# Performance work log

Measured on AMD Instinct MI355X. Metric: run time of the kernel, lower is better.

The kernel has to match this reference:

```python
import jax, jax.numpy as jnp
import numpy as np

N = 16384
F_IN = 256
F_OUT = 256


def setup_inputs() -> dict:
    key = jax.random.key(0)
    k1, k2, k3 = jax.random.split(key, 3)
    x = jax.random.normal(k1, (N, F_IN), dtype=jnp.float32)
    # dense 0/1 adjacency (original masks with adj[j] == 1)
    adj = jax.random.randint(k2, (N, N), 0, 2, dtype=jnp.int32)
    # glorot-uniform init for weight [2F_in, F_out]
    stdv = np.sqrt(6.0 / (2 * F_IN + F_OUT)).astype(np.float32)
    weight = jax.random.uniform(k3, (2 * F_IN, F_OUT), dtype=jnp.float32,
                                minval=-stdv, maxval=stdv)
    bias = jnp.zeros((F_OUT,), dtype=jnp.float32)
    return {"x": x, "adj": adj, "weight": weight, "bias": bias}


def reference(x, adj, weight, bias):
    # Mean over neighbors (adj row == 1): segment-mean expressed as a
    # normalized dense matmul -- equivalent to the per-row boolean-mask mean.
    a = adj.astype(x.dtype)                      # [N, N]
    deg = jnp.sum(a, axis=1, keepdims=True)      # [N, 1]
    x1 = (a @ x) / deg                           # [N, F] neighbor mean
    n_x = jnp.concatenate([x1, x], axis=1)       # [N, 2F]
    return n_x @ weight + bias                   # [N, F_out]
```

## Files before the change

### kernel.cpp

```cpp
#include <hip/hip_runtime.h>
#include <hip/hip_bf16.h>
#include <stdint.h>


typedef short bf16x8 __attribute__((ext_vector_type(8)));
typedef float f32x4  __attribute__((ext_vector_type(4)));

__device__ __forceinline__ uint32_t pack_bf16_rne(float lo, float hi) {
    uint32_t ul = __float_as_uint(lo);
    uint32_t uh = __float_as_uint(hi);
    ul = (ul + 0x7fffu + ((ul >> 16) & 1u)) >> 16;
    uh = (uh + 0x7fffu + ((uh >> 16) & 1u)) >> 16;
    return ul | (uh << 16);
}

__device__ __forceinline__ void gload_lds16(const void* g, void* l) {
    __builtin_amdgcn_global_load_lds(
        (__attribute__((address_space(1))) void*)g,
        (__attribute__((address_space(3))) void*)l, 16, 0, 0);
}

__global__ __launch_bounds__(256) void k_transpose_w(const float* __restrict__ w,
                                                     uint16_t* __restrict__ wt) {
    int idx = blockIdx.x * 256 + threadIdx.x;
    int n = idx >> 8;
    int k = idx & 255;
    int row = (n < 256) ? k : (256 + k);
    int col = (n < 256) ? n : (n - 256);
    uint32_t u = __float_as_uint(w[row * 256 + col]);
    u = (u + 0x7fffu + ((u >> 16) & 1u)) >> 16;
    wt[idx] = (uint16_t)u;
}

__global__ __launch_bounds__(256) void k_small_gemm(const float* __restrict__ x,
                                                    const uint16_t* __restrict__ wt,
                                                    const float* __restrict__ bias,
                                                    uint16_t* __restrict__ yT,
                                                    float* __restrict__ z) {
    __shared__ uint16_t As[128 * 32];
    __shared__ uint16_t Bs[128 * 32];

    const int t  = threadIdx.x;
    const int ct = blockIdx.x;
    const int rt = blockIdx.y;
    const int m0 = rt * 128;
    const int n0 = ct * 128;

    const int lane = t & 63, w = t >> 6;
    const int wr = w >> 1, wc = w & 1;
    const int l15 = lane & 15, quad = lane >> 4;

    f32x4 acc[4][4] = {};

    float4 a_reg[4];
    uint4  b_reg[2];

#pragma unroll
    for (int i = 0; i < 4; ++i) {
        int f4 = t + 256 * i, row = f4 >> 3, c4 = f4 & 7;
        a_reg[i] = *(const float4*)(x + (m0 + row) * 256 + c4 * 4);
    }
#pragma unroll
    for (int i = 0; i < 2; ++i) {
        int u4 = t + 256 * i, n_l = u4 >> 2, part = u4 & 3;
        b_reg[i] = *(const uint4*)(wt + (n0 + n_l) * 256 + part * 8);
    }

    for (int kk = 0; kk < 8; ++kk) {
        __syncthreads();
#pragma unroll
        for (int i = 0; i < 4; ++i) {
            int f4 = t + 256 * i, row = f4 >> 3, c4 = f4 & 7;
            uint2 p;
            p.x = pack_bf16_rne(a_reg[i].x, a_reg[i].y);
            p.y = pack_bf16_rne(a_reg[i].z, a_reg[i].w);
            *(uint2*)(As + row * 32 + c4 * 4) = p;
        }
#pragma unroll
        for (int i = 0; i < 2; ++i) {
            int u4 = t + 256 * i, n_l = u4 >> 2, part = u4 & 3;
            *(uint4*)(Bs + n_l * 32 + part * 8) = b_reg[i];
        }
        if (kk < 7) {
            int k0 = (kk + 1) * 32;
#pragma unroll
            for (int i = 0; i < 4; ++i) {
                int f4 = t + 256 * i, row = f4 >> 3, c4 = f4 & 7;
                a_reg[i] = *(const float4*)(x + (m0 + row) * 256 + k0 + c4 * 4);
            }
#pragma unroll
            for (int i = 0; i < 2; ++i) {
                int u4 = t + 256 * i, n_l = u4 >> 2, part = u4 & 3;
                b_reg[i] = *(const uint4*)(wt + (n0 + n_l) * 256 + k0 + part * 8);
            }
        }
        __syncthreads();

        bf16x8 a_frag[4], b_frag[4];
#pragma unroll
        for (int fr = 0; fr < 4; ++fr)
            a_frag[fr] = *(const bf16x8*)(As + (wr * 64 + fr * 16 + l15) * 32 + quad * 8);
#pragma unroll
        for (int fc = 0; fc < 4; ++fc)
            b_frag[fc] = *(const bf16x8*)(Bs + (wc * 64 + fc * 16 + l15) * 32 + quad * 8);
#pragma unroll
        for (int fr = 0; fr < 4; ++fr)
#pragma unroll
            for (int fc = 0; fc < 4; ++fc)
                acc[fr][fc] = __builtin_amdgcn_mfma_f32_16x16x32_bf16(
                    a_frag[fr], b_frag[fc], acc[fr][fc], 0, 0, 0);
    }

    if (ct < 2) {
#pragma unroll
        for (int fr = 0; fr < 4; ++fr) {
            int m_base = m0 + wr * 64 + fr * 16 + quad * 4;
#pragma unroll
            for (int fc = 0; fc < 4; ++fc) {
                int n_g = n0 + wc * 64 + fc * 16 + l15;
                uint2 pp;
                pp.x = pack_bf16_rne(acc[fr][fc][0], acc[fr][fc][1]);
                pp.y = pack_bf16_rne(acc[fr][fc][2], acc[fr][fc][3]);
                *(uint2*)(yT + (size_t)n_g * 16384 + m_base) = pp;
            }
        }
    } else {
#pragma unroll
        for (int fr = 0; fr < 4; ++fr) {
            int m_base = m0 + wr * 64 + fr * 16 + quad * 4;
#pragma unroll
            for (int fc = 0; fc < 4; ++fc) {
                int n_g = (n0 - 256) + wc * 64 + fc * 16 + l15;
                float bv = bias[n_g];
#pragma unroll
                for (int r = 0; r < 4; ++r)
                    z[(size_t)(m_base + r) * 256 + n_g] = acc[fr][fc][r] + bv;
            }
        }
    }
}

#define A_STRIDE 40
#define A_SZ (64 * A_STRIDE)
#define B_SZ (256 * 32)
#define KITER 256
__global__ __launch_bounds__(512, 4) void k_big_gemm(const int* __restrict__ adj,
                                                     const uint16_t* __restrict__ yT,
                                                     float* __restrict__ part,
                                                     int* __restrict__ degw) {
    __shared__ uint16_t As_f[2 * A_SZ];
    __shared__ uint16_t Bs_f[2 * B_SZ];

    const int t = threadIdx.x;
    const int m0 = blockIdx.x * 64;
    const int ky = blockIdx.y;
    const int kbase = ky * 8192;
    const int lane = t & 63, w = t >> 6;
    const int wr = w >> 2, wc = w & 3;
    const int l15 = lane & 15, quad = lane >> 4;

    f32x4 acc[2][4] = {};

    const int a_n = t >> 3, a_c4 = t & 7;
    const int4* pa4 = (const int4*)(adj + (size_t)(m0 + a_n) * 16384 + kbase) + a_c4;
    const int a_lds = a_n * A_STRIDE + a_c4 * 4;

    const uint16_t* pbg[2];
    int b_ldsbase[2];
#pragma unroll
    for (int i = 0; i < 2; ++i) {
        int base = (w * 2 + i) * 64;
        int s = base + lane;
        int bn = s >> 2;
        int bc = (s & 3) ^ ((bn >> 1) & 3);
        pbg[i] = yT + (size_t)bn * 16384 + kbase + bc * 8;
        b_ldsbase[i] = base * 8;
    }

    int4 aP = pa4[0];
    int4 aB = pa4[8];
    pa4 += 16;
#pragma unroll
    for (int i = 0; i < 2; ++i) {
        gload_lds16(pbg[i], &Bs_f[b_ldsbase[i]]);
        pbg[i] += 32;
    }
    int degp = aP.x + aP.y + aP.z + aP.w;
    {
        uint2 pv;
        pv.x = (uint32_t)(aP.x | (aP.y << 16)) * 0x3F80u;
        pv.y = (uint32_t)(aP.z | (aP.w << 16)) * 0x3F80u;
        *(uint2*)&As_f[a_lds] = pv;
    }
    __syncthreads();

    for (int kk = 0; kk < KITER; ++kk) {
        const int p = kk & 1;
        int4 aNew;
        if (kk < KITER - 2) { aNew = pa4[0]; pa4 += 8; }
        if (kk < KITER - 1) {
#pragma unroll
            for (int i = 0; i < 2; ++i) {
                gload_lds16(pbg[i], &Bs_f[(1 - p) * B_SZ + b_ldsbase[i]]);
                pbg[i] += 32;
            }
        }

        const uint16_t* Ar = As_f + p * A_SZ;
        const uint16_t* Br = Bs_f + p * B_SZ;
        bf16x8 af[2], bfr[4];
#pragma unroll
        for (int fr = 0; fr < 2; ++fr) {
            int row = wr * 32 + fr * 16 + l15;
            af[fr] = *(const bf16x8*)(Ar + row * A_STRIDE + quad * 8);
        }
#pragma unroll
        for (int fc = 0; fc < 4; ++fc) {
            int n = wc * 64 + fc * 16 + l15;
            int cs = quad ^ ((n >> 1) & 3);
            bfr[fc] = *(const bf16x8*)(Br + n * 32 + cs * 8);
        }
#pragma unroll
        for (int fr = 0; fr < 2; ++fr)
#pragma unroll
            for (int fc = 0; fc < 4; ++fc)
                acc[fr][fc] = __builtin_amdgcn_mfma_f32_16x16x32_bf16(
                    af[fr], bfr[fc], acc[fr][fc], 0, 0, 0);

        if (kk < KITER - 1) {
            degp += aB.x + aB.y + aB.z + aB.w;
            uint2 pv;
            pv.x = (uint32_t)(aB.x | (aB.y << 16)) * 0x3F80u;
            pv.y = (uint32_t)(aB.z | (aB.w << 16)) * 0x3F80u;
            *(uint2*)&As_f[(1 - p) * A_SZ + a_lds] = pv;
        }
        if (kk < KITER - 2) aB = aNew;
        __syncthreads();
    }

    degp += __shfl_down(degp, 4);
    degp += __shfl_down(degp, 2);
    degp += __shfl_down(degp, 1);
    if ((t & 7) == 0) degw[ky * 16384 + m0 + a_n] = degp;

    float* pc = part + (size_t)ky * 16384 * 256;
#pragma unroll
    for (int fr = 0; fr < 2; ++fr) {
#pragma unroll
        for (int r = 0; r < 4; ++r) {
            int m_l = wr * 32 + fr * 16 + quad * 4 + r;
            size_t mrow = (size_t)(m0 + m_l) * 256;
#pragma unroll
            for (int fc = 0; fc < 4; ++fc) {
                int n_g = wc * 64 + fc * 16 + l15;
                pc[mrow + n_g] = acc[fr][fc][r];
            }
        }
    }
}

__global__ __launch_bounds__(256) void k_reduce(const float* __restrict__ part,
                                                const int* __restrict__ degw,
                                                const float* __restrict__ z,
                                                float* __restrict__ out) {
    int i4 = blockIdx.x * 256 + threadIdx.x;
    int m = i4 >> 6;
    float4 p0 = ((const float4*)part)[i4];
    float4 p1 = ((const float4*)part)[i4 + 16384 * 64];
    float4 zz = ((const float4*)z)[i4];
    float inv = 1.0f / (float)(degw[m] + degw[16384 + m]);
    float4 o;
    o.x = (p0.x + p1.x) * inv + zz.x;
    o.y = (p0.y + p1.y) * inv + zz.y;
    o.z = (p0.z + p1.z) * inv + zz.z;
    o.w = (p0.w + p1.w) * inv + zz.w;
    ((float4*)out)[i4] = o;
}

extern "C" void kernel_launch(void* const* d_in, const int* in_sizes, int n_in,
                              void* d_out, int out_size, void* d_ws, size_t ws_size,
                              hipStream_t stream) {
    const float* x      = (const float*)d_in[0];
    const int*   adj    = (const int*)d_in[1];
    const float* weight = (const float*)d_in[2];
    const float* bias   = (const float*)d_in[3];
    float* out = (float*)d_out;

    uint16_t* wt   = (uint16_t*)d_ws;
    uint16_t* yT   = (uint16_t*)((char*)d_ws + 262144);
    float*    z    = (float*)((char*)d_ws + 262144 + 8388608);
    float*    partb= (float*)((char*)d_ws + 262144 + 8388608 + 16777216);
    int*      degw = (int*)((char*)d_ws + 262144 + 8388608 + 16777216 + 33554432);

    k_transpose_w<<<512, 256, 0, stream>>>(weight, wt);
    k_small_gemm<<<dim3(4, 128), 256, 0, stream>>>(x, wt, bias, yT, z);
    k_big_gemm<<<dim3(256, 2), 512, 0, stream>>>(adj, yT, partb, degw);
    k_reduce<<<4096, 256, 0, stream>>>(partb, degw, z, out);
}
```

Baseline: 1.487 ms.

## Triple-buffer big GEMM LDS stages with explicit waitcnt and barrier control

Replaces the double-buffered main loop of the adjacency GEMM with a three-stage LDS ring for both the packed adjacency tile and the yT tile. The loop is unrolled by three with a macro, and __syncthreads is replaced by a partial s_waitcnt vmcnt plus an explicit barrier, so global loads for stage k+2 can stay in flight while stage k is computed. This is meant to hide global-load latency better. The cost is 50% more LDS per block, which may lower occupancy under launch_bounds(512,4). The hand-written waitcnt counts are fragile and could race if the compiler reorders memory operations.

```diff
diff --git a/kernel.cpp b/kernel.cpp
--- a/kernel.cpp
+++ b/kernel.cpp
@@ -144,12 +144,51 @@
 #define A_SZ (64 * A_STRIDE)
 #define B_SZ (256 * 32)
 #define KITER 256
+
+#define BIG_STEP(CONS, PACK, ISSUE, KK)                                         \
+  do {                                                                          \
+    int4 aNew = aB;                                                             \
+    if ((KK) < KITER - 2) {                                                     \
+      aNew = pa4[0]; pa4 += 8;                                                  \
+      gload_lds16(pbg0, Bs##ISSUE + b_lb0); pbg0 += 32;                         \
+      gload_lds16(pbg1, Bs##ISSUE + b_lb1); pbg1 += 32;                         \
+    }                                                                           \
+       \
+    asm volatile("s_waitcnt vmcnt(3)" ::: "memory");                            \
+    if ((KK) < KITER - 1) {                                                     \
+      degp += aB.x + aB.y + aB.z + aB.w;                                        \
+      uint2 pv;                                                                 \
+      pv.x = (uint32_t)(aB.x | (aB.y << 16)) * 0x3F80u;                         \
+      pv.y = (uint32_t)(aB.z | (aB.w << 16)) * 0x3F80u;                         \
+      *(uint2*)&As##PACK[a_lds] = pv;                                           \
+      aB = aNew;                                                                \
+    }                                                                           \
+    {                                                                           \
+      bf16x8 af[2], bfr[4];                                                     \
+      _Pragma("unroll") for (int fr = 0; fr < 2; ++fr) {                        \
+        int row = wr * 32 + fr * 16 + l15;                                      \
+        af[fr] = *(const bf16x8*)(As##CONS + row * A_STRIDE + quad * 8);        \
+      }                                                                         \
+      _Pragma("unroll") for (int fc = 0; fc < 4; ++fc) {                        \
+        int n = wc * 64 + fc * 16 + l15;                                        \
+        int cs = quad ^ ((n >> 1) & 3);                                         \
+        bfr[fc] = *(const bf16x8*)(Bs##CONS + n * 32 + cs * 8);                 \
+      }                                                                         \
+      _Pragma("unroll") for (int fr = 0; fr < 2; ++fr)                          \
+        _Pragma("unroll") for (int fc = 0; fc < 4; ++fc)                        \
+          acc[fr][fc] = __builtin_amdgcn_mfma_f32_16x16x32_bf16(                \
+              af[fr], bfr[fc], acc[fr][fc], 0, 0, 0);                           \
+    }                                                                           \
+                             \
+    asm volatile("s_waitcnt lgkmcnt(0)\n\ts_barrier" ::: "memory");             \
+  } while (0)
+
 __global__ __launch_bounds__(512, 4) void k_big_gemm(const int* __restrict__ adj,
                                                      const uint16_t* __restrict__ yT,
                                                      float* __restrict__ part,
                                                      int* __restrict__ degw) {
-    __shared__ uint16_t As_f[2 * A_SZ];
-    __shared__ uint16_t Bs_f[2 * B_SZ];
+    __shared__ uint16_t As0[A_SZ], As1[A_SZ], As2[A_SZ];
+    __shared__ uint16_t Bs0[B_SZ], Bs1[B_SZ], Bs2[B_SZ];
 
     const int t = threadIdx.x;
     const int m0 = blockIdx.x * 64;
@@ -165,78 +204,43 @@
     const int4* pa4 = (const int4*)(adj + (size_t)(m0 + a_n) * 16384 + kbase) + a_c4;
     const int a_lds = a_n * A_STRIDE + a_c4 * 4;
 
-    const uint16_t* pbg[2];
-    int b_ldsbase[2];
-#pragma unroll
-    for (int i = 0; i < 2; ++i) {
-        int base = (w * 2 + i) * 64;
-        int s = base + lane;
-        int bn = s >> 2;
-        int bc = (s & 3) ^ ((bn >> 1) & 3);
-        pbg[i] = yT + (size_t)bn * 16384 + kbase + bc * 8;
-        b_ldsbase[i] = base * 8;
-    }
-
-    int4 aP = pa4[0];
+    const uint16_t *pbg0, *pbg1;
+    int b_lb0, b_lb1;
+    {
+        int base0 = (w * 2 + 0) * 64, base1 = (w * 2 + 1) * 64;
+        int s0 = base0 + lane, s1 = base1 + lane;
+        int bn0 = s0 >> 2, bn1 = s1 >> 2;
+        int bc0 = (s0 & 3) ^ ((bn0 >> 1) & 3);
+        int bc1 = (s1 & 3) ^ ((bn1 >> 1) & 3);
+        pbg0 = yT + (size_t)bn0 * 16384 + kbase + bc0 * 8;
+        pbg1 = yT + (size_t)bn1 * 16384 + kbase + bc1 * 8;
+        b_lb0 = base0 * 8;
+        b_lb1 = base1 * 8;
+    }
+
+    gload_lds16(pbg0, Bs0 + b_lb0); pbg0 += 32;
+    gload_lds16(pbg1, Bs0 + b_lb1); pbg1 += 32;
+    int4 a0 = pa4[0];
+    gload_lds16(pbg0, Bs1 + b_lb0); pbg0 += 32;
+    gload_lds16(pbg1, Bs1 + b_lb1); pbg1 += 32;
     int4 aB = pa4[8];
     pa4 += 16;
-#pragma unroll
-    for (int i = 0; i < 2; ++i) {
-        gload_lds16(pbg[i], &Bs_f[b_ldsbase[i]]);
-        pbg[i] += 32;
-    }
-    int degp = aP.x + aP.y + aP.z + aP.w;
+    asm volatile("s_waitcnt vmcnt(2)" ::: "memory");
+    int degp = a0.x + a0.y + a0.z + a0.w;
     {
         uint2 pv;
-        pv.x = (uint32_t)(aP.x | (aP.y << 16)) * 0x3F80u;
-        pv.y = (uint32_t)(aP.z | (aP.w << 16)) * 0x3F80u;
-        *(uint2*)&As_f[a_lds] = pv;
-    }
-    __syncthreads();
-
-    for (int kk = 0; kk < KITER; ++kk) {
-        const int p = kk & 1;
-        int4 aNew;
-        if (kk < KITER - 2) { aNew = pa4[0]; pa4 += 8; }
-        if (kk < KITER - 1) {
-#pragma unroll
-            for (int i = 0; i < 2; ++i) {
-                gload_lds16(pbg[i], &Bs_f[(1 - p) * B_SZ + b_ldsbase[i]]);
-                pbg[i] += 32;
-            }
-        }
-
-        const uint16_t* Ar = As_f + p * A_SZ;
-        const uint16_t* Br = Bs_f + p * B_SZ;
-        bf16x8 af[2], bfr[4];
-#pragma unroll
-        for (int fr = 0; fr < 2; ++fr) {
-            int row = wr * 32 + fr * 16 + l15;
-            af[fr] = *(const bf16x8*)(Ar + row * A_STRIDE + quad * 8);
-        }
-#pragma unroll
-        for (int fc = 0; fc < 4; ++fc) {
-            int n = wc * 64 + fc * 16 + l15;
-            int cs = quad ^ ((n >> 1) & 3);
-            bfr[fc] = *(const bf16x8*)(Br + n * 32 + cs * 8);
-        }
-#pragma unroll
-        for (int fr = 0; fr < 2; ++fr)
-#pragma unroll
-            for (int fc = 0; fc < 4; ++fc)
-                acc[fr][fc] = __builtin_amdgcn_mfma_f32_16x16x32_bf16(
-                    af[fr], bfr[fc], acc[fr][fc], 0, 0, 0);
-
-        if (kk < KITER - 1) {
-            degp += aB.x + aB.y + aB.z + aB.w;
-            uint2 pv;
-            pv.x = (uint32_t)(aB.x | (aB.y << 16)) * 0x3F80u;
-            pv.y = (uint32_t)(aB.z | (aB.w << 16)) * 0x3F80u;
-            *(uint2*)&As_f[(1 - p) * A_SZ + a_lds] = pv;
-        }
-        if (kk < KITER - 2) aB = aNew;
-        __syncthreads();
-    }
+        pv.x = (uint32_t)(a0.x | (a0.y << 16)) * 0x3F80u;
+        pv.y = (uint32_t)(a0.z | (a0.w << 16)) * 0x3F80u;
+        *(uint2*)&As0[a_lds] = pv;
+    }
+    asm volatile("s_waitcnt lgkmcnt(0)\n\ts_barrier" ::: "memory");
+
+    for (int kk = 0; kk < KITER - 1; kk += 3) {
+        BIG_STEP(0, 1, 2, kk);
+        BIG_STEP(1, 2, 0, kk + 1);
+        BIG_STEP(2, 0, 1, kk + 2);
+    }
+    BIG_STEP(0, 1, 2, KITER - 1);
 
     degp += __shfl_down(degp, 4);
     degp += __shfl_down(degp, 2);
```

New measurement: 1.501 ms. No clear change (+0.9%).
